# Optimization experiments

Hardware: AMD Instinct MI355X
Metric: run time of the kernel (lower is better)

## Reference

```python
import jax, jax.numpy as jnp
import numpy as np


def _mlp(x, w1, b1, w2, b2):
    # x: [b,s,h]; w1: [h,f]; w2: [f,h]
    h = jax.nn.gelu(jnp.einsum('bsh,hf->bsf', x, w1) + b1, approximate=False)
    return jnp.einsum('bsf,fh->bsh', h, w2) + b2


def setup_inputs() -> dict:
    key = jax.random.key(0)
    ks = jax.random.split(key, 8)
    B, S, H, F, E, NS = 4, 1024, 1024, 2048, 8, 2
    sc_in = 1.0 / np.sqrt(H)
    sc_hid = 1.0 / np.sqrt(F)
    return {
        'x': jax.random.normal(ks[0], (B, S, H), jnp.float32),
        'shared_w1': jax.random.normal(ks[1], (NS, H, F), jnp.float32) * sc_in,
        'shared_b1': jnp.zeros((NS, F), jnp.float32),
        'shared_w2': jax.random.normal(ks[2], (NS, F, H), jnp.float32) * sc_hid,
        'shared_b2': jnp.zeros((NS, H), jnp.float32),
        'exp_w1': jax.random.normal(ks[3], (E, H, F), jnp.float32) * sc_in,
        'exp_b1': jnp.zeros((E, F), jnp.float32),
        'exp_w2': jax.random.normal(ks[4], (E, F, H), jnp.float32) * sc_hid,
        'exp_b2': jnp.zeros((E, H), jnp.float32),
        'router_w': jax.random.normal(ks[5], (H, E), jnp.float32) * sc_in,
        'router_b': jnp.zeros((E,), jnp.float32),
        'top_k': 2,
    }


def reference(x, shared_w1, shared_b1, shared_w2, shared_b2,
              exp_w1, exp_b1, exp_w2, exp_b2, router_w, router_b, top_k):
    E = exp_w1.shape[0]
    # shared experts: always active, summed
    share_out = jnp.zeros_like(x)
    for n in range(shared_w1.shape[0]):
        share_out = share_out + _mlp(x, shared_w1[n], shared_b1[n], shared_w2[n], shared_b2[n])

    # router: softmax + topk indices per token
    logits = jnp.einsum('bsh,he->bse', x, router_w) + router_b
    scores = jax.nn.softmax(logits, axis=-1)
    _, top_idx = jax.lax.top_k(scores, top_k)          # [b,s,k]
    mask = jax.nn.one_hot(top_idx, E, dtype=x.dtype).sum(axis=-2)  # [b,s,E]

    # routed experts: compute all, combine with top-k mask (unweighted, per source)
    hid = jax.nn.gelu(jnp.einsum('bsh,ehf->ebsf', x, exp_w1) + exp_b1[:, None, None, :],
                      approximate=False)
    exp_out = jnp.einsum('ebsf,efh->ebsh', hid, exp_w2) + exp_b2[:, None, None, :]
    routed = jnp.einsum('ebsh,bse->bsh', exp_out, mask)

    return share_out + routed
```

## Files before the change

### kernel.cpp

```cpp
#include <hip/hip_runtime.h>
#include <hip/hip_bf16.h>

#define T_TOK 4096
#define HD    1024
#define FD    2048
#define NEXP  8
#define NSH   2

using u16 = unsigned short;
typedef __bf16 bf16x8 __attribute__((ext_vector_type(8)));
typedef float  f32x4  __attribute__((ext_vector_type(4)));
typedef u16    u16x2  __attribute__((ext_vector_type(2)));
typedef u16    u16x4  __attribute__((ext_vector_type(4)));

__device__ __forceinline__ u16 f2bf(float f) {
    __hip_bfloat16 h = __float2bfloat16(f);
    u16 u; __builtin_memcpy(&u, &h, 2);
    return u;
}
__device__ __forceinline__ float bf2f(u16 u) {
    unsigned v = ((unsigned)u) << 16;
    float f; __builtin_memcpy(&f, &v, 4);
    return f;
}

__device__ __forceinline__ void gl2lds16(const u16* g, u16* l) {
    __builtin_amdgcn_global_load_lds((__attribute__((address_space(1))) void*)(g),
                                     (__attribute__((address_space(3))) void*)(l),
                                     16, 0, 0);
}

__device__ __forceinline__ void gemm_k_loop(
    const u16* a0, const u16* a1, const u16* b0, const u16* b1,
    u16* As, u16* Bs, int kIters, f32x4 acc[4][4])
{
    const int tid  = threadIdx.x;
    const int wave = tid >> 6, lane = tid & 63;
    const int wm = wave >> 1, wn = wave & 1;
    const int l16 = lane & 15, quad = lane >> 4;
    u16* lA0 = As + (wave * 32 + 0)  * 32 + lane * 8;
    u16* lA1 = As + (wave * 32 + 16) * 32 + lane * 8;
    u16* lB0 = Bs + (wave * 32 + 0)  * 32 + lane * 8;
    u16* lB1 = Bs + (wave * 32 + 16) * 32 + lane * 8;

    for (int kt = 0; kt < kIters; ++kt) {
        gl2lds16(a0, lA0);
        gl2lds16(a1, lA1);
        gl2lds16(b0, lB0);
        gl2lds16(b1, lB1);
        a0 += 32; a1 += 32; b0 += 32; b1 += 32;
        __syncthreads();
        bf16x8 af[4], bfv[4];
#pragma unroll
        for (int i = 0; i < 4; ++i)
            af[i] = *(const bf16x8*)(As + (wm * 64 + i * 16 + l16) * 32 + quad * 8);
#pragma unroll
        for (int j = 0; j < 4; ++j)
            bfv[j] = *(const bf16x8*)(Bs + (wn * 64 + j * 16 + l16) * 32 + quad * 8);
#pragma unroll
        for (int i = 0; i < 4; ++i)
#pragma unroll
            for (int j = 0; j < 4; ++j)
                acc[i][j] = __builtin_amdgcn_mfma_f32_16x16x32_bf16(af[i], bfv[j], acc[i][j], 0, 0, 0);
        __syncthreads();
    }
}

__device__ __forceinline__ float gelu_fast(float v) {
    float u = v * (0.7978845608028654f + 0.035677408136300125f * v * v);
    return v * __builtin_amdgcn_rcpf(1.0f + __expf(-2.0f * u));
}

#define EPI_STRIDE 66
template<bool GELU>
__device__ __forceinline__ void epi_store_bf16(
    f32x4 acc[4][4], const float bj[4],
    u16* __restrict__ dst, size_t ld, int rowbase, int colbase, u16* lds)
{
    const int lane = threadIdx.x & 63;
    const int l16 = lane & 15, quad = lane >> 4;
    const int rr = lane >> 2, seg = lane & 3;
#pragma unroll
    for (int i = 0; i < 4; ++i) {
#pragma unroll
        for (int j = 0; j < 4; ++j)
#pragma unroll
            for (int r = 0; r < 4; ++r) {
                float v = acc[i][j][r] + bj[j];
                if (GELU) v = gelu_fast(v);
                lds[(quad * 4 + r) * EPI_STRIDE + j * 16 + l16] = f2bf(v);
            }
        __asm__ volatile("s_waitcnt lgkmcnt(0)" ::: "memory");
        const u16* lp = lds + rr * EPI_STRIDE + seg * 16;
        u16x4 v0 = *(const u16x4*)(lp);
        u16x4 v1 = *(const u16x4*)(lp + 4);
        u16x4 v2 = *(const u16x4*)(lp + 8);
        u16x4 v3 = *(const u16x4*)(lp + 12);
        u16* gp = dst + (size_t)(rowbase + i * 16 + rr) * ld + colbase + seg * 16;
        *(u16x4*)(gp)      = v0;
        *(u16x4*)(gp + 4)  = v1;
        *(u16x4*)(gp + 8)  = v2;
        *(u16x4*)(gp + 12) = v3;
        __asm__ volatile("s_waitcnt lgkmcnt(0)" ::: "memory");
    }
}

template<int NX, int CX, int CY>
__device__ __forceinline__ void xcd_map2d(int& nt, int& mt) {
    const int flat = blockIdx.x + NX * blockIdx.y;
    const int xcd = flat & 7, idx = flat >> 3;
    nt = (xcd & 3) * CX + idx % CX;
    mt = (xcd >> 2) * CY + (idx / CX) % CY;
}

__global__ __launch_bounds__(256) void router_convert_kernel(
    const float* __restrict__ x, const float* __restrict__ rw, const float* __restrict__ rb,
    u16* __restrict__ xb, int* __restrict__ cnt, int* __restrict__ lists, int* __restrict__ pos)
{
    const int t = blockIdx.x * 4 + (threadIdx.x >> 6);
    const int lane = threadIdx.x & 63;
    const float* xr = x + (size_t)t * HD;
    u16* xbr = xb + (size_t)t * HD;
    float acc[NEXP];
#pragma unroll
    for (int e = 0; e < NEXP; ++e) acc[e] = 0.f;
#pragma unroll
    for (int it = 0; it < 4; ++it) {
        int h0 = it * 256 + lane * 4;
        float4 v = *(const float4*)(xr + h0);
        ushort4 o = { f2bf(v.x), f2bf(v.y), f2bf(v.z), f2bf(v.w) };
        *(ushort4*)(xbr + h0) = o;
        float xv[4] = { v.x, v.y, v.z, v.w };
#pragma unroll
        for (int q = 0; q < 4; ++q) {
            const float4* wp = (const float4*)(rw + (size_t)(h0 + q) * NEXP);
            float4 w0 = wp[0], w1 = wp[1];
            acc[0] += xv[q] * w0.x; acc[1] += xv[q] * w0.y;
            acc[2] += xv[q] * w0.z; acc[3] += xv[q] * w0.w;
            acc[4] += xv[q] * w1.x; acc[5] += xv[q] * w1.y;
            acc[6] += xv[q] * w1.z; acc[7] += xv[q] * w1.w;
        }
    }
#pragma unroll
    for (int e = 0; e < NEXP; ++e)
        for (int off = 32; off; off >>= 1) acc[e] += __shfl_xor(acc[e], off, 64);
    if (lane == 0) {
#pragma unroll
        for (int e = 0; e < NEXP; ++e) acc[e] += rb[e];
        int b1i = 0;
        for (int e = 1; e < NEXP; ++e) if (acc[e] > acc[b1i]) b1i = e;
        int b2i = (b1i == 0) ? 1 : 0;
        for (int e = 0; e < NEXP; ++e) if (e != b1i && acc[e] > acc[b2i]) b2i = e;
        int p1 = atomicAdd(&cnt[b1i], 1); lists[b1i * T_TOK + p1] = t;
        int p2 = atomicAdd(&cnt[b2i], 1); lists[b2i * T_TOK + p2] = t;
        pos[2 * t]     = (b1i << 13) | p1;
        pos[2 * t + 1] = (b2i << 13) | p2;
    }
}

__global__ void offsets_kernel(const int* __restrict__ cnt, int* __restrict__ pfx) {
    if (threadIdx.x == 0 && blockIdx.x == 0) {
        int s = 0;
        for (int e = 0; e < NEXP; ++e) { pfx[e] = s; s += ((cnt[e] + 127) >> 7) << 7; }
        pfx[NEXP] = s;
    }
}

__global__ __launch_bounds__(256) void transpose_w1_kernel(
    const float* __restrict__ sw1, const float* __restrict__ ew1, u16* __restrict__ wt)
{
    __shared__ u16 tile[32][65];
    const int z = blockIdx.z;
    const float* src = (z < NSH) ? (sw1 + (size_t)z * HD * FD)
                                 : (ew1 + (size_t)(z - NSH) * HD * FD);
    u16* dst = wt + (size_t)z * FD * HD;
    const int tx = threadIdx.x, ty = threadIdx.y;
    const int c0 = blockIdx.x * 32;
    const int r0 = blockIdx.y * 64;
#pragma unroll
    for (int k = 0; k < 8; ++k)
        tile[tx][ty + 8 * k] = f2bf(src[(size_t)(r0 + ty + 8 * k) * FD + c0 + tx]);
    __syncthreads();
#pragma unroll
    for (int k = 0; k < 4; ++k) {
        int c = ty + 8 * k;
        u16x2 v = { tile[c][2 * tx], tile[c][2 * tx + 1] };
        *(u16x2*)(dst + (size_t)(c0 + c) * HD + r0 + 2 * tx) = v;
    }
}

__global__ __launch_bounds__(256) void transpose_w2_kernel(
    const float* __restrict__ sw2, const float* __restrict__ ew2, u16* __restrict__ wt)
{
    __shared__ u16 tile[32][65];
    const int z = blockIdx.z;
    const float* src; u16* dst; size_t ldd;
    if (z < NSH) { src = sw2 + (size_t)z * FD * HD; dst = wt + (size_t)z * FD; ldd = 2 * FD; }
    else { src = ew2 + (size_t)(z - NSH) * FD * HD;
           dst = wt + (size_t)NSH * FD * HD + (size_t)(z - NSH) * HD * FD; ldd = FD; }
    const int tx = threadIdx.x, ty = threadIdx.y;
    const int c0 = blockIdx.x * 32;
    const int r0 = blockIdx.y * 64;
#pragma unroll
    for (int k = 0; k < 8; ++k)
        tile[tx][ty + 8 * k] = f2bf(src[(size_t)(r0 + ty + 8 * k) * HD + c0 + tx]);
    __syncthreads();
#pragma unroll
    for (int k = 0; k < 4; ++k) {
        int c = ty + 8 * k;
        u16x2 v = { tile[c][2 * tx], tile[c][2 * tx + 1] };
        *(u16x2*)(dst + (size_t)(c0 + c) * ldd + r0 + 2 * tx) = v;
    }
}

__global__ __launch_bounds__(256, 4) void gemm1_all_kernel(
    const u16* __restrict__ xb, const u16* __restrict__ w1t,
    const float* __restrict__ sb1, const float* __restrict__ eb1,
    const int* __restrict__ cnt, const int* __restrict__ pfx,
    const int* __restrict__ lists,
    u16* __restrict__ hidS, u16* __restrict__ hidE)
{
    const int z = blockIdx.z;
    const bool routed = (z >= NSH);
    const int e = z - NSH;
    int nt, mt;
    if (!routed) xcd_map2d<FD / 128, 4, 16>(nt, mt);
    else { nt = blockIdx.x; mt = blockIdx.y; }
    if (routed && mt * 128 >= cnt[e]) return;
    __shared__ __align__(16) u16 S[2 * 128 * 32];
    u16* As = S;
    u16* Bs = S + 128 * 32;
    const int tid = threadIdx.x, wave = tid >> 6, lane = tid & 63;
    const int r0 = wave * 32 + (lane >> 2), ch = (lane & 3) * 8;
    const u16 *a0, *a1;
    if (routed) {
        int tok0 = lists[e * T_TOK + mt * 128 + r0];
        int tok1 = lists[e * T_TOK + mt * 128 + r0 + 16];
        a0 = xb + (size_t)tok0 * HD + ch;
        a1 = xb + (size_t)tok1 * HD + ch;
    } else {
        a0 = xb + (size_t)(mt * 128 + r0) * HD + ch;
        a1 = a0 + (size_t)16 * HD;
    }
    const u16* b0 = w1t + (size_t)z * FD * HD + (size_t)(nt * 128 + r0) * HD + ch;
    const u16* b1 = b0 + (size_t)16 * HD;
    f32x4 acc[4][4] = {};
    gemm_k_loop(a0, a1, b0, b1, As, Bs, HD / 32, acc);

    const int wm = wave >> 1, wn = wave & 1, l16 = lane & 15;
    const float* bias = routed ? (eb1 + e * FD) : (sb1 + z * FD);
    float bj[4];
#pragma unroll
    for (int j = 0; j < 4; ++j) bj[j] = bias[nt * 128 + wn * 64 + j * 16 + l16];
    u16* dst   = routed ? hidE : hidS;
    const size_t ld = routed ? FD : 2 * FD;
    const int rowbase = (routed ? (pfx[e] + mt * 128) : (mt * 128)) + wm * 64;
    const int colbase = (routed ? 0 : z * FD) + nt * 128 + wn * 64;
    epi_store_bf16<true>(acc, bj, dst, ld, rowbase, colbase, S + wave * 16 * EPI_STRIDE);
}

__global__ __launch_bounds__(256, 4) void gemm2_all_kernel(
    const u16* __restrict__ hidS, const u16* __restrict__ hidE,
    const u16* __restrict__ w2t,
    const float* __restrict__ sb2, const float* __restrict__ eb2,
    const int* __restrict__ cnt, const int* __restrict__ pfx,
    float* __restrict__ out, u16* __restrict__ routedOut)
{
    const int z = blockIdx.z;
    const int e = z - 1;
    int nt, mt;
    if (z == 0) xcd_map2d<HD / 128, 2, 16>(nt, mt);
    else { nt = blockIdx.x; mt = blockIdx.y; }
    if (z >= 1 && mt * 128 >= cnt[e]) return;
    __shared__ __align__(16) u16 S[2 * 128 * 32];
    u16* As = S;
    u16* Bs = S + 128 * 32;
    const int tid = threadIdx.x, wave = tid >> 6, lane = tid & 63;
    const int r0 = wave * 32 + (lane >> 2), ch = (lane & 3) * 8;
    const int wm = wave >> 1, wn = wave & 1, l16 = lane & 15, quad = lane >> 4;
    f32x4 acc[4][4] = {};

    if (z == 0) {
        const u16* a0 = hidS + (size_t)(mt * 128 + r0) * (2 * FD) + ch;
        const u16* a1 = a0 + (size_t)16 * (2 * FD);
        const u16* b0 = w2t + (size_t)(nt * 128 + r0) * (2 * FD) + ch;
        const u16* b1 = b0 + (size_t)16 * (2 * FD);
        gemm_k_loop(a0, a1, b0, b1, As, Bs, (2 * FD) / 32, acc);
#pragma unroll
        for (int j = 0; j < 4; ++j) {
            int h = nt * 128 + wn * 64 + j * 16 + l16;
            float bv = sb2[h] + sb2[HD + h];
#pragma unroll
            for (int i = 0; i < 4; ++i) {
                int row = mt * 128 + wm * 64 + i * 16 + quad * 4;
#pragma unroll
                for (int r = 0; r < 4; ++r)
                    out[(size_t)(row + r) * HD + h] = acc[i][j][r] + bv;
            }
        }
    } else {
        const int base = pfx[e];
        const u16* a0 = hidE + (size_t)(base + mt * 128 + r0) * FD + ch;
        const u16* a1 = a0 + (size_t)16 * FD;
        const u16* b0 = w2t + (size_t)NSH * FD * HD + (size_t)e * HD * FD
                            + (size_t)(nt * 128 + r0) * FD + ch;
        const u16* b1 = b0 + (size_t)16 * FD;
        gemm_k_loop(a0, a1, b0, b1, As, Bs, FD / 32, acc);
        float bj[4];
#pragma unroll
        for (int j = 0; j < 4; ++j) bj[j] = eb2[e * HD + nt * 128 + wn * 64 + j * 16 + l16];
        epi_store_bf16<false>(acc, bj, routedOut, HD,
                              base + mt * 128 + wm * 64, nt * 128 + wn * 64,
                              S + wave * 16 * EPI_STRIDE);
    }
}

__global__ __launch_bounds__(256, 4) void gemm2_routed_atomic_kernel(
    const u16* __restrict__ hidE, const u16* __restrict__ w2t,
    const float* __restrict__ eb2, const int* __restrict__ cnt,
    const int* __restrict__ pfx, const int* __restrict__ lists,
    float* __restrict__ out)
{
    const int e = blockIdx.z, nt = blockIdx.x, mt = blockIdx.y;
    const int n_e = cnt[e];
    if (mt * 128 >= n_e) return;
    __shared__ __align__(16) u16 S[2 * 128 * 32];
    u16* As = S;
    u16* Bs = S + 128 * 32;
    const int tid = threadIdx.x, wave = tid >> 6, lane = tid & 63;
    const int r0 = wave * 32 + (lane >> 2), ch = (lane & 3) * 8;
    const int base = pfx[e];
    const u16* a0 = hidE + (size_t)(base + mt * 128 + r0) * FD + ch;
    const u16* a1 = a0 + (size_t)16 * FD;
    const u16* b0 = w2t + (size_t)NSH * FD * HD + (size_t)e * HD * FD
                        + (size_t)(nt * 128 + r0) * FD + ch;
    const u16* b1 = b0 + (size_t)16 * FD;
    f32x4 acc[4][4] = {};
    gemm_k_loop(a0, a1, b0, b1, As, Bs, FD / 32, acc);
    const int wm = wave >> 1, wn = wave & 1, l16 = lane & 15, quad = lane >> 4;
#pragma unroll
    for (int j = 0; j < 4; ++j) {
        int h = nt * 128 + wn * 64 + j * 16 + l16;
        float bv = eb2[e * HD + h];
#pragma unroll
        for (int i = 0; i < 4; ++i) {
            int local = mt * 128 + wm * 64 + i * 16 + quad * 4;
#pragma unroll
            for (int r = 0; r < 4; ++r)
                if (local + r < n_e) {
                    int t = lists[e * T_TOK + local + r];
                    atomicAdd(&out[(size_t)t * HD + h], acc[i][j][r] + bv);
                }
        }
    }
}

__global__ __launch_bounds__(256) void finalize_kernel(
    const u16* __restrict__ routedOut, const int* __restrict__ pos,
    const int* __restrict__ pfx, float* __restrict__ out)
{
    const int t = blockIdx.x;
    int enc0 = pos[2 * t], enc1 = pos[2 * t + 1];
    int row0 = pfx[enc0 >> 13] + (enc0 & 8191);
    int row1 = pfx[enc1 >> 13] + (enc1 & 8191);
    int h = threadIdx.x * 4;
    ushort4 a = *(const ushort4*)(routedOut + (size_t)row0 * HD + h);
    ushort4 b = *(const ushort4*)(routedOut + (size_t)row1 * HD + h);
    float* po = out + (size_t)t * HD + h;
    float4 o = *(const float4*)po;
    o.x += bf2f(a.x) + bf2f(b.x);
    o.y += bf2f(a.y) + bf2f(b.y);
    o.z += bf2f(a.z) + bf2f(b.z);
    o.w += bf2f(a.w) + bf2f(b.w);
    *(float4*)po = o;
}

extern "C" void kernel_launch(void* const* d_in, const int* in_sizes, int n_in,
                              void* d_out, int out_size, void* d_ws, size_t ws_size,
                              hipStream_t stream)
{
    (void)in_sizes; (void)n_in; (void)out_size;
    const float* x   = (const float*)d_in[0];
    const float* sw1 = (const float*)d_in[1];
    const float* sb1 = (const float*)d_in[2];
    const float* sw2 = (const float*)d_in[3];
    const float* sb2 = (const float*)d_in[4];
    const float* ew1 = (const float*)d_in[5];
    const float* eb1 = (const float*)d_in[6];
    const float* ew2 = (const float*)d_in[7];
    const float* eb2 = (const float*)d_in[8];
    const float* rw  = (const float*)d_in[9];
    const float* rb  = (const float*)d_in[10];
    float* out = (float*)d_out;

    const bool plain = (ws_size >= (size_t)132284544);
    char* ws   = (char*)d_ws;
    u16*  wt   = (u16*)ws;
    u16*  hidS = (u16*)(ws + 41943040);
    u16*  hidE = (u16*)(ws + 75497472);
    u16*  xb   = (u16*)(ws + 113246208);
    u16*  rOut = (u16*)(ws + 113246208);
    size_t smallOfs = plain ? (size_t)132120576 : (size_t)121634816;
    int*  cnt   = (int*)(ws + smallOfs);
    int*  pfx   = (int*)(ws + smallOfs + 64);
    int*  lists = (int*)(ws + smallOfs + 128);
    int*  pos   = (int*)(ws + smallOfs + 128 + NEXP * T_TOK * 4);

    hipMemsetAsync(cnt, 0, 128 + (size_t)NEXP * T_TOK * 4, stream);

    router_convert_kernel<<<dim3(T_TOK / 4), dim3(256), 0, stream>>>(x, rw, rb, xb, cnt, lists, pos);
    offsets_kernel<<<dim3(1), dim3(64), 0, stream>>>(cnt, pfx);
    transpose_w1_kernel<<<dim3(FD / 32, HD / 64, NSH + NEXP), dim3(32, 8), 0, stream>>>(sw1, ew1, wt);

    gemm1_all_kernel<<<dim3(FD / 128, T_TOK / 128, NSH + NEXP), dim3(256), 0, stream>>>(
        xb, wt, sb1, eb1, cnt, pfx, lists, hidS, hidE);

    transpose_w2_kernel<<<dim3(HD / 32, FD / 64, NSH + NEXP), dim3(32, 8), 0, stream>>>(sw2, ew2, wt);

    if (plain) {
        gemm2_all_kernel<<<dim3(HD / 128, T_TOK / 128, 1 + NEXP), dim3(256), 0, stream>>>(
            hidS, hidE, wt, sb2, eb2, cnt, pfx, out, rOut);
        finalize_kernel<<<dim3(T_TOK), dim3(256), 0, stream>>>(rOut, pos, pfx, out);
    } else {
        gemm2_all_kernel<<<dim3(HD / 128, T_TOK / 128, 1), dim3(256), 0, stream>>>(
            hidS, hidE, wt, sb2, eb2, cnt, pfx, out, rOut);
        gemm2_routed_atomic_kernel<<<dim3(HD / 128, T_TOK / 128, NEXP), dim3(256), 0, stream>>>(
            hidE, wt, eb2, cnt, pfx, lists, out);
    }
}
```

Measured before the change: 530.5 us.

## Double-buffer LDS tiles and XOR-swizzle chunks to overlap loads and cut bank conflicts

```diff
diff --git a/kernel.cpp b/kernel.cpp
--- a/kernel.cpp
+++ b/kernel.cpp
@@ -32,31 +32,40 @@
 
 __device__ __forceinline__ void gemm_k_loop(
     const u16* a0, const u16* a1, const u16* b0, const u16* b1,
-    u16* As, u16* Bs, int kIters, f32x4 acc[4][4])
+    u16* S, int kIters, f32x4 acc[4][4])
 {
     const int tid  = threadIdx.x;
     const int wave = tid >> 6, lane = tid & 63;
     const int wm = wave >> 1, wn = wave & 1;
     const int l16 = lane & 15, quad = lane >> 4;
-    u16* lA0 = As + (wave * 32 + 0)  * 32 + lane * 8;
-    u16* lA1 = As + (wave * 32 + 16) * 32 + lane * 8;
-    u16* lB0 = Bs + (wave * 32 + 0)  * 32 + lane * 8;
-    u16* lB1 = Bs + (wave * 32 + 16) * 32 + lane * 8;
-
+    const int xs = (l16 >> 1) & 3;
+    const int dA0 = (wave * 32 + 0)  * 32 + lane * 8;
+    const int dA1 = (wave * 32 + 16) * 32 + lane * 8;
+    gl2lds16(a0, S + dA0);
+    gl2lds16(a1, S + dA1);
+    gl2lds16(b0, S + 4096 + dA0);
+    gl2lds16(b1, S + 4096 + dA1);
+    a0 += 32; a1 += 32; b0 += 32; b1 += 32;
+    __syncthreads();
     for (int kt = 0; kt < kIters; ++kt) {
-        gl2lds16(a0, lA0);
-        gl2lds16(a1, lA1);
-        gl2lds16(b0, lB0);
-        gl2lds16(b1, lB1);
-        a0 += 32; a1 += 32; b0 += 32; b1 += 32;
-        __syncthreads();
+        const int cur = kt & 1;
+        u16* Sn = S + (cur ^ 1) * 8192;
+        if (kt + 1 < kIters) {
+            gl2lds16(a0, Sn + dA0);
+            gl2lds16(a1, Sn + dA1);
+            gl2lds16(b0, Sn + 4096 + dA0);
+            gl2lds16(b1, Sn + 4096 + dA1);
+            a0 += 32; a1 += 32; b0 += 32; b1 += 32;
+        }
+        const u16* As = S + cur * 8192;
+        const u16* Bs = As + 4096;
         bf16x8 af[4], bfv[4];
 #pragma unroll
         for (int i = 0; i < 4; ++i)
-            af[i] = *(const bf16x8*)(As + (wm * 64 + i * 16 + l16) * 32 + quad * 8);
+            af[i] = *(const bf16x8*)(As + (wm * 64 + i * 16 + l16) * 32 + ((quad ^ xs) * 8));
 #pragma unroll
         for (int j = 0; j < 4; ++j)
-            bfv[j] = *(const bf16x8*)(Bs + (wn * 64 + j * 16 + l16) * 32 + quad * 8);
+            bfv[j] = *(const bf16x8*)(Bs + (wn * 64 + j * 16 + l16) * 32 + ((quad ^ xs) * 8));
 #pragma unroll
         for (int i = 0; i < 4; ++i)
 #pragma unroll
@@ -227,11 +236,10 @@
     if (!routed) xcd_map2d<FD / 128, 4, 16>(nt, mt);
     else { nt = blockIdx.x; mt = blockIdx.y; }
     if (routed && mt * 128 >= cnt[e]) return;
-    __shared__ __align__(16) u16 S[2 * 128 * 32];
-    u16* As = S;
-    u16* Bs = S + 128 * 32;
+    __shared__ __align__(16) u16 S[4 * 4096];
     const int tid = threadIdx.x, wave = tid >> 6, lane = tid & 63;
-    const int r0 = wave * 32 + (lane >> 2), ch = (lane & 3) * 8;
+    const int r0 = wave * 32 + (lane >> 2);
+    const int ch = ((lane & 3) ^ ((lane >> 3) & 3)) * 8;
     const u16 *a0, *a1;
     if (routed) {
         int tok0 = lists[e * T_TOK + mt * 128 + r0];
@@ -245,7 +253,7 @@
     const u16* b0 = w1t + (size_t)z * FD * HD + (size_t)(nt * 128 + r0) * HD + ch;
     const u16* b1 = b0 + (size_t)16 * HD;
     f32x4 acc[4][4] = {};
-    gemm_k_loop(a0, a1, b0, b1, As, Bs, HD / 32, acc);
+    gemm_k_loop(a0, a1, b0, b1, S, HD / 32, acc);
 
     const int wm = wave >> 1, wn = wave & 1, l16 = lane & 15;
     const float* bias = routed ? (eb1 + e * FD) : (sb1 + z * FD);
@@ -272,11 +280,10 @@
     if (z == 0) xcd_map2d<HD / 128, 2, 16>(nt, mt);
     else { nt = blockIdx.x; mt = blockIdx.y; }
     if (z >= 1 && mt * 128 >= cnt[e]) return;
-    __shared__ __align__(16) u16 S[2 * 128 * 32];
-    u16* As = S;
-    u16* Bs = S + 128 * 32;
+    __shared__ __align__(16) u16 S[4 * 4096];
     const int tid = threadIdx.x, wave = tid >> 6, lane = tid & 63;
-    const int r0 = wave * 32 + (lane >> 2), ch = (lane & 3) * 8;
+    const int r0 = wave * 32 + (lane >> 2);
+    const int ch = ((lane & 3) ^ ((lane >> 3) & 3)) * 8;
     const int wm = wave >> 1, wn = wave & 1, l16 = lane & 15, quad = lane >> 4;
     f32x4 acc[4][4] = {};
 
@@ -285,7 +292,7 @@
         const u16* a1 = a0 + (size_t)16 * (2 * FD);
         const u16* b0 = w2t + (size_t)(nt * 128 + r0) * (2 * FD) + ch;
         const u16* b1 = b0 + (size_t)16 * (2 * FD);
-        gemm_k_loop(a0, a1, b0, b1, As, Bs, (2 * FD) / 32, acc);
+        gemm_k_loop(a0, a1, b0, b1, S, (2 * FD) / 32, acc);
 #pragma unroll
         for (int j = 0; j < 4; ++j) {
             int h = nt * 128 + wn * 64 + j * 16 + l16;
@@ -305,7 +312,7 @@
         const u16* b0 = w2t + (size_t)NSH * FD * HD + (size_t)e * HD * FD
                             + (size_t)(nt * 128 + r0) * FD + ch;
         const u16* b1 = b0 + (size_t)16 * FD;
-        gemm_k_loop(a0, a1, b0, b1, As, Bs, FD / 32, acc);
+        gemm_k_loop(a0, a1, b0, b1, S, FD / 32, acc);
         float bj[4];
 #pragma unroll
         for (int j = 0; j < 4; ++j) bj[j] = eb2[e * HD + nt * 128 + wn * 64 + j * 16 + l16];
@@ -324,11 +331,10 @@
     const int e = blockIdx.z, nt = blockIdx.x, mt = blockIdx.y;
     const int n_e = cnt[e];
     if (mt * 128 >= n_e) return;
-    __shared__ __align__(16) u16 S[2 * 128 * 32];
-    u16* As = S;
-    u16* Bs = S + 128 * 32;
+    __shared__ __align__(16) u16 S[4 * 4096];
     const int tid = threadIdx.x, wave = tid >> 6, lane = tid & 63;
-    const int r0 = wave * 32 + (lane >> 2), ch = (lane & 3) * 8;
+    const int r0 = wave * 32 + (lane >> 2);
+    const int ch = ((lane & 3) ^ ((lane >> 3) & 3)) * 8;
     const int base = pfx[e];
     const u16* a0 = hidE + (size_t)(base + mt * 128 + r0) * FD + ch;
     const u16* a1 = a0 + (size_t)16 * FD;
@@ -336,7 +342,7 @@
                         + (size_t)(nt * 128 + r0) * FD + ch;
     const u16* b1 = b0 + (size_t)16 * FD;
     f32x4 acc[4][4] = {};
-    gemm_k_loop(a0, a1, b0, b1, As, Bs, FD / 32, acc);
+    gemm_k_loop(a0, a1, b0, b1, S, FD / 32, acc);
     const int wm = wave >> 1, wn = wave & 1, l16 = lane & 15, quad = lane >> 4;
 #pragma unroll
     for (int j = 0; j < 4; ++j) {
```

Measured after the change: 527.2 us. Within noise of the previous version (-0.6%).

## Double-buffer LDS with BK=64 and XOR-swizzled layout in all GEMM kernels

Applied to the files above, without the earlier changes.

```diff
diff --git a/kernel.cpp b/kernel.cpp
--- a/kernel.cpp
+++ b/kernel.cpp
@@ -30,38 +30,62 @@
                                      16, 0, 0);
 }
 
-__device__ __forceinline__ void gemm_k_loop(
-    const u16* a0, const u16* a1, const u16* b0, const u16* b1,
-    u16* As, u16* Bs, int kIters, f32x4 acc[4][4])
+__device__ __forceinline__ void stage8(
+    const u16*& a0, const u16*& a1, const u16*& a2, const u16*& a3,
+    const u16*& b0, const u16*& b1, const u16*& b2, const u16*& b3,
+    u16* T, int dst0)
+{
+    gl2lds16(a0, T + dst0);
+    gl2lds16(a1, T + dst0 + 512);
+    gl2lds16(a2, T + dst0 + 1024);
+    gl2lds16(a3, T + dst0 + 1536);
+    gl2lds16(b0, T + 8192 + dst0);
+    gl2lds16(b1, T + 8192 + dst0 + 512);
+    gl2lds16(b2, T + 8192 + dst0 + 1024);
+    gl2lds16(b3, T + 8192 + dst0 + 1536);
+    a0 += 64; a1 += 64; a2 += 64; a3 += 64;
+    b0 += 64; b1 += 64; b2 += 64; b3 += 64;
+}
+
+__device__ __forceinline__ void gemm_k_loop64(
+    const u16* a0, const u16* a1, const u16* a2, const u16* a3,
+    const u16* b0, const u16* b1, const u16* b2, const u16* b3,
+    u16* S, int kIters, f32x4 acc[4][4])
 {
     const int tid  = threadIdx.x;
     const int wave = tid >> 6, lane = tid & 63;
     const int wm = wave >> 1, wn = wave & 1;
     const int l16 = lane & 15, quad = lane >> 4;
-    u16* lA0 = As + (wave * 32 + 0)  * 32 + lane * 8;
-    u16* lA1 = As + (wave * 32 + 16) * 32 + lane * 8;
-    u16* lB0 = Bs + (wave * 32 + 0)  * 32 + lane * 8;
-    u16* lB1 = Bs + (wave * 32 + 16) * 32 + lane * 8;
-
+    const int x3 = l16 & 7;
+    const int dst0 = (wave * 32) * 64 + lane * 8;
+
+    stage8(a0, a1, a2, a3, b0, b1, b2, b3, S, dst0);
+    __syncthreads();
     for (int kt = 0; kt < kIters; ++kt) {
-        gl2lds16(a0, lA0);
-        gl2lds16(a1, lA1);
-        gl2lds16(b0, lB0);
-        gl2lds16(b1, lB1);
-        a0 += 32; a1 += 32; b0 += 32; b1 += 32;
-        __syncthreads();
-        bf16x8 af[4], bfv[4];
-#pragma unroll
-        for (int i = 0; i < 4; ++i)
-            af[i] = *(const bf16x8*)(As + (wm * 64 + i * 16 + l16) * 32 + quad * 8);
-#pragma unroll
-        for (int j = 0; j < 4; ++j)
-            bfv[j] = *(const bf16x8*)(Bs + (wn * 64 + j * 16 + l16) * 32 + quad * 8);
-#pragma unroll
-        for (int i = 0; i < 4; ++i)
+        u16* cur = S + (kt & 1) * 16384;
+        if (kt + 1 < kIters) {
+            u16* nx = S + ((kt + 1) & 1) * 16384;
+            stage8(a0, a1, a2, a3, b0, b1, b2, b3, nx, dst0);
+        }
+        const u16* As = cur;
+        const u16* Bs = cur + 8192;
+#pragma unroll
+        for (int kk = 0; kk < 2; ++kk) {
+            bf16x8 af[4], bfv[4];
+#pragma unroll
+            for (int i = 0; i < 4; ++i)
+                af[i] = *(const bf16x8*)(As + (wm * 64 + i * 16 + l16) * 64
+                                            + ((((kk << 2) | quad) ^ x3) * 8));
 #pragma unroll
             for (int j = 0; j < 4; ++j)
-                acc[i][j] = __builtin_amdgcn_mfma_f32_16x16x32_bf16(af[i], bfv[j], acc[i][j], 0, 0, 0);
+                bfv[j] = *(const bf16x8*)(Bs + (wn * 64 + j * 16 + l16) * 64
+                                             + ((((kk << 2) | quad) ^ x3) * 8));
+#pragma unroll
+            for (int i = 0; i < 4; ++i)
+#pragma unroll
+                for (int j = 0; j < 4; ++j)
+                    acc[i][j] = __builtin_amdgcn_mfma_f32_16x16x32_bf16(af[i], bfv[j], acc[i][j], 0, 0, 0);
+        }
         __syncthreads();
     }
 }
@@ -213,7 +237,7 @@
     }
 }
 
-__global__ __launch_bounds__(256, 4) void gemm1_all_kernel(
+__global__ __launch_bounds__(256, 2) void gemm1_all_kernel(
     const u16* __restrict__ xb, const u16* __restrict__ w1t,
     const float* __restrict__ sb1, const float* __restrict__ eb1,
     const int* __restrict__ cnt, const int* __restrict__ pfx,
@@ -227,25 +251,31 @@
     if (!routed) xcd_map2d<FD / 128, 4, 16>(nt, mt);
     else { nt = blockIdx.x; mt = blockIdx.y; }
     if (routed && mt * 128 >= cnt[e]) return;
-    __shared__ __align__(16) u16 S[2 * 128 * 32];
-    u16* As = S;
-    u16* Bs = S + 128 * 32;
+    __shared__ __align__(16) u16 S[2 * 16384];
     const int tid = threadIdx.x, wave = tid >> 6, lane = tid & 63;
-    const int r0 = wave * 32 + (lane >> 2), ch = (lane & 3) * 8;
-    const u16 *a0, *a1;
+    const int rsel = wave * 32 + (lane >> 3);
+    const int ch = ((tid & 7) ^ ((tid >> 3) & 7)) * 8;
+    const u16 *a0, *a1, *a2, *a3;
     if (routed) {
-        int tok0 = lists[e * T_TOK + mt * 128 + r0];
-        int tok1 = lists[e * T_TOK + mt * 128 + r0 + 16];
-        a0 = xb + (size_t)tok0 * HD + ch;
-        a1 = xb + (size_t)tok1 * HD + ch;
+        int tq[4];
+#pragma unroll
+        for (int q = 0; q < 4; ++q) tq[q] = lists[e * T_TOK + mt * 128 + rsel + q * 8];
+        a0 = xb + (size_t)tq[0] * HD + ch;
+        a1 = xb + (size_t)tq[1] * HD + ch;
+        a2 = xb + (size_t)tq[2] * HD + ch;
+        a3 = xb + (size_t)tq[3] * HD + ch;
     } else {
-        a0 = xb + (size_t)(mt * 128 + r0) * HD + ch;
-        a1 = a0 + (size_t)16 * HD;
-    }
-    const u16* b0 = w1t + (size_t)z * FD * HD + (size_t)(nt * 128 + r0) * HD + ch;
-    const u16* b1 = b0 + (size_t)16 * HD;
+        a0 = xb + (size_t)(mt * 128 + rsel) * HD + ch;
+        a1 = a0 + (size_t)8 * HD;
+        a2 = a0 + (size_t)16 * HD;
+        a3 = a0 + (size_t)24 * HD;
+    }
+    const u16* b0 = w1t + (size_t)z * FD * HD + (size_t)(nt * 128 + rsel) * HD + ch;
+    const u16* b1 = b0 + (size_t)8 * HD;
+    const u16* b2 = b0 + (size_t)16 * HD;
+    const u16* b3 = b0 + (size_t)24 * HD;
     f32x4 acc[4][4] = {};
-    gemm_k_loop(a0, a1, b0, b1, As, Bs, HD / 32, acc);
+    gemm_k_loop64(a0, a1, a2, a3, b0, b1, b2, b3, S, HD / 64, acc);
 
     const int wm = wave >> 1, wn = wave & 1, l16 = lane & 15;
     const float* bias = routed ? (eb1 + e * FD) : (sb1 + z * FD);
@@ -259,7 +289,7 @@
     epi_store_bf16<true>(acc, bj, dst, ld, rowbase, colbase, S + wave * 16 * EPI_STRIDE);
 }
 
-__global__ __launch_bounds__(256, 4) void gemm2_all_kernel(
+__global__ __launch_bounds__(256, 2) void gemm2_all_kernel(
     const u16* __restrict__ hidS, const u16* __restrict__ hidE,
     const u16* __restrict__ w2t,
     const float* __restrict__ sb2, const float* __restrict__ eb2,
@@ -272,20 +302,23 @@
     if (z == 0) xcd_map2d<HD / 128, 2, 16>(nt, mt);
     else { nt = blockIdx.x; mt = blockIdx.y; }
     if (z >= 1 && mt * 128 >= cnt[e]) return;
-    __shared__ __align__(16) u16 S[2 * 128 * 32];
-    u16* As = S;
-    u16* Bs = S + 128 * 32;
+    __shared__ __align__(16) u16 S[2 * 16384];
     const int tid = threadIdx.x, wave = tid >> 6, lane = tid & 63;
-    const int r0 = wave * 32 + (lane >> 2), ch = (lane & 3) * 8;
+    const int rsel = wave * 32 + (lane >> 3);
+    const int ch = ((tid & 7) ^ ((tid >> 3) & 7)) * 8;
     const int wm = wave >> 1, wn = wave & 1, l16 = lane & 15, quad = lane >> 4;
     f32x4 acc[4][4] = {};
 
     if (z == 0) {
-        const u16* a0 = hidS + (size_t)(mt * 128 + r0) * (2 * FD) + ch;
-        const u16* a1 = a0 + (size_t)16 * (2 * FD);
-        const u16* b0 = w2t + (size_t)(nt * 128 + r0) * (2 * FD) + ch;
-        const u16* b1 = b0 + (size_t)16 * (2 * FD);
-        gemm_k_loop(a0, a1, b0, b1, As, Bs, (2 * FD) / 32, acc);
+        const u16* a0 = hidS + (size_t)(mt * 128 + rsel) * (2 * FD) + ch;
+        const u16* a1 = a0 + (size_t)8 * (2 * FD);
+        const u16* a2 = a0 + (size_t)16 * (2 * FD);
+        const u16* a3 = a0 + (size_t)24 * (2 * FD);
+        const u16* b0 = w2t + (size_t)(nt * 128 + rsel) * (2 * FD) + ch;
+        const u16* b1 = b0 + (size_t)8 * (2 * FD);
+        const u16* b2 = b0 + (size_t)16 * (2 * FD);
+        const u16* b3 = b0 + (size_t)24 * (2 * FD);
+        gemm_k_loop64(a0, a1, a2, a3, b0, b1, b2, b3, S, (2 * FD) / 64, acc);
 #pragma unroll
         for (int j = 0; j < 4; ++j) {
             int h = nt * 128 + wn * 64 + j * 16 + l16;
@@ -300,12 +333,16 @@
         }
     } else {
         const int base = pfx[e];
-        const u16* a0 = hidE + (size_t)(base + mt * 128 + r0) * FD + ch;
-        const u16* a1 = a0 + (size_t)16 * FD;
+        const u16* a0 = hidE + (size_t)(base + mt * 128 + rsel) * FD + ch;
+        const u16* a1 = a0 + (size_t)8 * FD;
+        const u16* a2 = a0 + (size_t)16 * FD;
+        const u16* a3 = a0 + (size_t)24 * FD;
         const u16* b0 = w2t + (size_t)NSH * FD * HD + (size_t)e * HD * FD
-                            + (size_t)(nt * 128 + r0) * FD + ch;
-        const u16* b1 = b0 + (size_t)16 * FD;
-        gemm_k_loop(a0, a1, b0, b1, As, Bs, FD / 32, acc);
+                            + (size_t)(nt * 128 + rsel) * FD + ch;
+        const u16* b1 = b0 + (size_t)8 * FD;
+        const u16* b2 = b0 + (size_t)16 * FD;
+        const u16* b3 = b0 + (size_t)24 * FD;
+        gemm_k_loop64(a0, a1, a2, a3, b0, b1, b2, b3, S, FD / 64, acc);
         float bj[4];
 #pragma unroll
         for (int j = 0; j < 4; ++j) bj[j] = eb2[e * HD + nt * 128 + wn * 64 + j * 16 + l16];
@@ -315,7 +352,7 @@
     }
 }
 
-__global__ __launch_bounds__(256, 4) void gemm2_routed_atomic_kernel(
+__global__ __launch_bounds__(256, 2) void gemm2_routed_atomic_kernel(
     const u16* __restrict__ hidE, const u16* __restrict__ w2t,
     const float* __restrict__ eb2, const int* __restrict__ cnt,
     const int* __restrict__ pfx, const int* __restrict__ lists,
@@ -324,19 +361,22 @@
     const int e = blockIdx.z, nt = blockIdx.x, mt = blockIdx.y;
     const int n_e = cnt[e];
     if (mt * 128 >= n_e) return;
-    __shared__ __align__(16) u16 S[2 * 128 * 32];
-    u16* As = S;
-    u16* Bs = S + 128 * 32;
+    __shared__ __align__(16) u16 S[2 * 16384];
     const int tid = threadIdx.x, wave = tid >> 6, lane = tid & 63;
-    const int r0 = wave * 32 + (lane >> 2), ch = (lane & 3) * 8;
+    const int rsel = wave * 32 + (lane >> 3);
+    const int ch = ((tid & 7) ^ ((tid >> 3) & 7)) * 8;
     const int base = pfx[e];
-    const u16* a0 = hidE + (size_t)(base + mt * 128 + r0) * FD + ch;
-    const u16* a1 = a0 + (size_t)16 * FD;
+    const u16* a0 = hidE + (size_t)(base + mt * 128 + rsel) * FD + ch;
+    const u16* a1 = a0 + (size_t)8 * FD;
+    const u16* a2 = a0 + (size_t)16 * FD;
+    const u16* a3 = a0 + (size_t)24 * FD;
     const u16* b0 = w2t + (size_t)NSH * FD * HD + (size_t)e * HD * FD
-                        + (size_t)(nt * 128 + r0) * FD + ch;
-    const u16* b1 = b0 + (size_t)16 * FD;
+                        + (size_t)(nt * 128 + rsel) * FD + ch;
+    const u16* b1 = b0 + (size_t)8 * FD;
+    const u16* b2 = b0 + (size_t)16 * FD;
+    const u16* b3 = b0 + (size_t)24 * FD;
     f32x4 acc[4][4] = {};
-    gemm_k_loop(a0, a1, b0, b1, As, Bs, FD / 32, acc);
+    gemm_k_loop64(a0, a1, a2, a3, b0, b1, b2, b3, S, FD / 64, acc);
     const int wm = wave >> 1, wn = wave & 1, l16 = lane & 15, quad = lane >> 4;
 #pragma unroll
     for (int j = 0; j < 4; ++j) {
```

Result: faster. 503.8 us (-5.0%).
